# Kernel optimization log

Measured on AMD Instinct MI355X. Metric: run time of the kernel, lower is better.

The kernel has to match this reference:

```python
import jax, jax.numpy as jnp
import numpy as np

B = 65536          # number of 9-node graphs
NPG = 9            # nodes per graph (hardcoded in module)
N = B * NPG
D_IN, D_H = 11, 64
SOFTPLUS_BIAS = float(np.log(np.expm1(1.0)))  # biased_softplus_1.0 bias
SCALE_LB = 1e-4


def _make_edges():
    # fully connected (no self loops) within each 9-node graph
    pairs = np.array([(i, j) for i in range(NPG) for j in range(NPG) if i != j],
                     dtype=np.int64)  # [72, 2]
    offs = (np.arange(B, dtype=np.int64) * NPG)[:, None]
    src = (offs + pairs[None, :, 0]).ravel()
    dst = (offs + pairs[None, :, 1]).ravel()
    return jnp.asarray(np.stack([src, dst]))  # [2, E]


def setup_inputs() -> dict:
    key = jax.random.key(0)
    ks = jax.random.split(key, 12)
    s_in = 1.0 / np.sqrt(D_IN)
    s_h = 1.0 / np.sqrt(D_H)
    return {
        "x": jax.random.normal(ks[0], (N, D_IN), jnp.float32),
        "edge_index": _make_edges(),
        "W_in": jax.random.normal(ks[1], (D_H, D_IN), jnp.float32) * s_in,
        "b_in": jax.random.normal(ks[2], (D_H,), jnp.float32) * s_in,
        "W1_rel": jax.random.normal(ks[3], (D_H, D_H), jnp.float32) * s_h,
        "b1": jax.random.normal(ks[4], (D_H,), jnp.float32) * s_h,
        "W1_root": jax.random.normal(ks[5], (D_H, D_H), jnp.float32) * s_h,
        "W2_rel": jax.random.normal(ks[6], (D_H, D_H), jnp.float32) * s_h,
        "b2": jax.random.normal(ks[7], (D_H,), jnp.float32) * s_h,
        "W2_root": jax.random.normal(ks[8], (D_H, D_H), jnp.float32) * s_h,
        "W_head": jax.random.normal(ks[9], (8, D_H, 2), jnp.float32) * s_h,
        "b_head": jax.random.normal(ks[10], (8, 2), jnp.float32) * s_h,
    }


def _graph_conv(x, src, dst, W_rel, b_rel, W_root, n):
    # PyG GraphConv: lin_rel(sum_{j in N(i)} x_j) + lin_root(x_i)
    agg = jax.ops.segment_sum(x[src], dst, num_segments=n)  # scatter-add gather
    return agg @ W_rel.T + b_rel + x @ W_root.T


def reference(x, edge_index, W_in, b_in, W1_rel, b1, W1_root,
              W2_rel, b2, W2_root, W_head, b_head):
    n = x.shape[0]
    src, dst = edge_index[0], edge_index[1]
    h = x @ W_in.T + b_in                                   # [N, 64]
    h = jnp.tanh(_graph_conv(h, src, dst, W1_rel, b1, W1_root, n))
    h = jnp.tanh(_graph_conv(h, src, dst, W2_rel, b2, W2_root, n))
    hg = h.reshape(n // NPG, NPG, D_H)[:, 1:, :]            # drop node 0: [B, 8, 64]
    out = jnp.einsum('bnd,ndo->bno', hg, W_head) + b_head   # per-node head: [B, 8, 2]
    loc = out[..., 0]
    scale = jnp.maximum(jax.nn.softplus(out[..., 1] + SOFTPLUS_BIAS), SCALE_LB)
    return (loc, scale)
```

## Files before the change

kernel.cpp:

```cpp
#include <hip/hip_runtime.h>
#include <hip/hip_bf16.h>

#define NPG 9
#define DH 64
#define DIN 11
#define GPB 32
#define ROWS (GPB*NPG)
#define TPB 576
#define NGRAPH 65536
#define NBLK (NGRAPH/GPB)
#define OUT_HALF ((long long)NGRAPH*8)

typedef __attribute__((ext_vector_type(8))) short short8;
typedef __attribute__((ext_vector_type(4))) float f32x4;

__device__ float g_winT[DIN*DH];
__device__ short g_bfrag1[16*512];
__device__ short g_bfrag2[16*512];
__device__ short g_bfragH[2*512];

__device__ __forceinline__ short f2b(float f) {
  unsigned u = __builtin_bit_cast(unsigned, f);
  u += 0x7fffu + ((u >> 16) & 1u);
  return (short)(u >> 16);
}
__device__ __forceinline__ float b2f(short s) {
  unsigned u = ((unsigned)(unsigned short)s) << 16;
  return __builtin_bit_cast(float, u);
}
__device__ __forceinline__ float fast_tanh(float v) {
  float e = __expf(2.f*v);
  return 1.f - 2.f*__builtin_amdgcn_rcpf(e + 1.f);
}

__global__ void prep_kernel(const float* __restrict__ W_in,
                            const float* __restrict__ W1_rel, const float* __restrict__ W1_root,
                            const float* __restrict__ W2_rel, const float* __restrict__ W2_root,
                            const float* __restrict__ W_head) {
  int idx = blockIdx.x*blockDim.x + threadIdx.x;
  if (idx < DIN*DH) {
    int k = idx >> 6, f = idx & 63;
    g_winT[idx] = W_in[f*DIN + k];
  }
  if (idx < 16*512) {
    int frag = idx >> 9, kk = frag >> 2, nt = frag & 3;
    int l = (idx >> 3) & 63, j = idx & 7;
    int k2 = kk*32 + ((l >> 4) << 3) + j;
    int n  = nt*16 + (l & 15);
    float v1, v2;
    if (k2 < 64) {
      v1 = W1_root[n*DH + k2] - W1_rel[n*DH + k2];
      v2 = W2_root[n*DH + k2] - W2_rel[n*DH + k2];
    } else {
      v1 = W1_rel[n*DH + k2 - 64];
      v2 = W2_rel[n*DH + k2 - 64];
    }
    g_bfrag1[idx] = f2b(v1);
    g_bfrag2[idx] = f2b(v2);
  }
  if (idx < 2*512) {
    int kk = idx >> 9;
    int l = (idx >> 3) & 63, j = idx & 7;
    int k = kk*32 + ((l >> 4) << 3) + j;
    int n = l & 15;
    g_bfragH[idx] = f2b(W_head[(n >> 1)*(DH*2) + k*2 + (n & 1)]);
  }
}

#define HS_OFF(r, c) ((r)*64 + (((c) ^ ((r) & 7)) << 3))

__global__ __launch_bounds__(TPB) void fused_kernel(
    const float* __restrict__ x,
    const float* __restrict__ b_in,
    const float* __restrict__ b1,
    const float* __restrict__ b2,
    const float* __restrict__ bhead,
    float* __restrict__ out)
{
  __shared__ short Hs[ROWS*64];
  __shared__ union { float xs[ROWS*13]; short ss[GPB*64]; } u;

  const int tid  = threadIdx.x;
  const int lane = tid & 63;
  const int wave = tid >> 6;
  const int l15  = lane & 15;
  const int kgrp = lane >> 4;

  {
    const float* __restrict__ xsrc = x + (size_t)blockIdx.x * (ROWS*DIN);
    for (int i = tid; i < ROWS*DIN; i += TPB) {
      int r = (int)(((unsigned)i * 2979u) >> 15);
      int c = i - r*DIN;
      u.xs[r*13 + c] = xsrc[i];
    }
  }
  __syncthreads();

  if (tid < ROWS) {
    const int row = tid;
    float xr[DIN];
    #pragma unroll
    for (int k = 0; k < DIN; ++k) xr[k] = u.xs[row*13 + k];
    float z[DH];
    #pragma unroll
    for (int f = 0; f < DH; ++f) z[f] = b_in[f];
    #pragma unroll
    for (int k = 0; k < DIN; ++k) {
      const float s = xr[k];
      const float* __restrict__ w = &g_winT[k*DH];
      #pragma unroll
      for (int f = 0; f < DH; ++f) z[f] += s * w[f];
    }
    #pragma unroll
    for (int c = 0; c < 8; ++c) {
      short8 v;
      #pragma unroll
      for (int j = 0; j < 8; ++j) v[j] = f2b(z[c*8 + j]);
      *(short8*)&Hs[HS_OFF(row, c)] = v;
    }
  }
  __syncthreads();

  auto layer = [&](const short* __restrict__ bfrag, const float* __restrict__ bias) {
    if (tid < 256) {
      const int g = tid >> 3, fc = tid & 7;
      float s[8] = {0,0,0,0,0,0,0,0};
      #pragma unroll
      for (int j = 0; j < NPG; ++j) {
        const int r = g*NPG + j;
        short8 v = *(const short8*)&Hs[HS_OFF(r, fc)];
        #pragma unroll
        for (int e = 0; e < 8; ++e) s[e] += b2f(v[e]);
      }
      short8 o;
      #pragma unroll
      for (int e = 0; e < 8; ++e) o[e] = f2b(s[e]);
      *(short8*)&u.ss[g*64 + ((fc ^ (g & 7)) << 3)] = o;
    }
    __syncthreads();

    short8 B[4][4];
    #pragma unroll
    for (int kk = 0; kk < 4; ++kk)
      #pragma unroll
      for (int nt = 0; nt < 4; ++nt)
        B[kk][nt] = *(const short8*)&bfrag[((kk << 2) + nt)*512 + lane*8];

    float bias_c[4];
    #pragma unroll
    for (int nt = 0; nt < 4; ++nt) bias_c[nt] = bias[nt*16 + l15];

    f32x4 acc[2][4];
    #pragma unroll
    for (int tt = 0; tt < 2; ++tt)
      #pragma unroll
      for (int nt = 0; nt < 4; ++nt) acc[tt][nt] = (f32x4){0.f,0.f,0.f,0.f};

    #pragma unroll
    for (int tt = 0; tt < 2; ++tt) {
      const int row = (2*wave + tt)*16 + l15;
      const int g   = (row*57) >> 9;
      short8 A[4];
      #pragma unroll
      for (int kk = 0; kk < 2; ++kk)
        A[kk] = *(const short8*)&Hs[HS_OFF(row, kk*4 + kgrp)];
      #pragma unroll
      for (int kk = 2; kk < 4; ++kk)
        A[kk] = *(const short8*)&u.ss[g*64 + ((((kk - 2)*4 + kgrp) ^ (g & 7)) << 3)];
      #pragma unroll
      for (int kk = 0; kk < 4; ++kk)
        #pragma unroll
        for (int nt = 0; nt < 4; ++nt)
          acc[tt][nt] = __builtin_amdgcn_mfma_f32_16x16x32_bf16(A[kk], B[kk][nt], acc[tt][nt], 0, 0, 0);
    }
    __syncthreads();

    #pragma unroll
    for (int tt = 0; tt < 2; ++tt) {
      #pragma unroll
      for (int nt = 0; nt < 4; ++nt) {
        #pragma unroll
        for (int reg = 0; reg < 4; ++reg) {
          const int row = (2*wave + tt)*16 + kgrp*4 + reg;
          const int col = nt*16 + l15;
          float v = acc[tt][nt][reg] + bias_c[nt];
          v = fast_tanh(v);
          Hs[row*64 + (((col >> 3) ^ (row & 7)) << 3) + (col & 7)] = f2b(v);
        }
      }
    }
    __syncthreads();
  };

  layer(g_bfrag1, b1);
  layer(g_bfrag2, b2);

  short8 HB[2];
  #pragma unroll
  for (int kk = 0; kk < 2; ++kk)
    HB[kk] = *(const short8*)&g_bfragH[kk*512 + lane*8];

  const int p  = l15 >> 1;
  const int oc = l15 & 1;
  const float bh = bhead[p*2 + oc];

  #pragma unroll
  for (int tt = 0; tt < 2; ++tt) {
    const int t = 2*wave + tt;
    const int arow = t*16 + l15;
    f32x4 hacc = (f32x4){0.f,0.f,0.f,0.f};
    #pragma unroll
    for (int kk = 0; kk < 2; ++kk) {
      short8 A = *(const short8*)&Hs[HS_OFF(arow, kk*4 + kgrp)];
      hacc = __builtin_amdgcn_mfma_f32_16x16x32_bf16(A, HB[kk], hacc, 0, 0, 0);
    }
    #pragma unroll
    for (int reg = 0; reg < 4; ++reg) {
      const int row = t*16 + kgrp*4 + reg;
      const int g   = (row*57) >> 9;
      const int nn  = row - g*NPG;
      if (nn == p + 1) {
        const float v = hacc[reg] + bh;
        const long long gg = (long long)blockIdx.x * GPB + g;
        if (oc == 0) {
          out[gg*8 + p] = v;
        } else {
          float tv = v + 0.5413248546129181f;
          float e  = __expf(tv);
          float sp = (tv > 15.f) ? tv : __logf(1.f + e);
          out[OUT_HALF + gg*8 + p] = fmaxf(sp, 1e-4f);
        }
      }
    }
  }
}

extern "C" void kernel_launch(void* const* d_in, const int* in_sizes, int n_in,
                              void* d_out, int out_size, void* d_ws, size_t ws_size,
                              hipStream_t stream) {
  const float* x       = (const float*)d_in[0];
  const float* W_in    = (const float*)d_in[2];
  const float* b_in    = (const float*)d_in[3];
  const float* W1_rel  = (const float*)d_in[4];
  const float* b1      = (const float*)d_in[5];
  const float* W1_root = (const float*)d_in[6];
  const float* W2_rel  = (const float*)d_in[7];
  const float* b2      = (const float*)d_in[8];
  const float* W2_root = (const float*)d_in[9];
  const float* Whead   = (const float*)d_in[10];
  const float* bhead   = (const float*)d_in[11];
  float* out = (float*)d_out;

  hipLaunchKernelGGL(prep_kernel, dim3(32), dim3(256), 0, stream,
                     W_in, W1_rel, W1_root, W2_rel, W2_root, Whead);
  hipLaunchKernelGGL(fused_kernel, dim3(NBLK), dim3(TPB), 0, stream,
                     x, b_in, b1, b2, bhead, out);
}
```

Measured before the change: 227.2 us.

## Fold input projection into layer-1 weights and shrink blocks to 256 threads

Precomputes combined weights so the input linear layer and the first graph convolution collapse into one small MFMA on the 11-dim raw features plus per-graph feature sums, with a folded bias. This removes the per-row scalar 11x64 FMA projection and the first 64-dim aggregation. Blocks change to 28 graphs with 256 threads and launch bounds for four blocks per CU, with tail guards because 65536 is not divisible by 28. The prep kernel now runs as a single block doing serial 64-term dot products, and the input features are rounded to bf16 before the folded product, which may cost some accuracy.

```diff
diff --git a/kernel.cpp b/kernel.cpp
--- a/kernel.cpp
+++ b/kernel.cpp
@@ -4,25 +4,26 @@
 #define NPG 9
 #define DH 64
 #define DIN 11
-#define GPB 32
+#define GPB 28
 #define ROWS (GPB*NPG)
-#define TPB 576
+#define TPB 256
 #define NGRAPH 65536
-#define NBLK (NGRAPH/GPB)
+#define NROWTOT (NGRAPH*NPG)
+#define NBLK ((NGRAPH + GPB - 1)/GPB)
 #define OUT_HALF ((long long)NGRAPH*8)
 
 typedef __attribute__((ext_vector_type(8))) short short8;
+typedef __attribute__((ext_vector_type(4))) short short4v;
 typedef __attribute__((ext_vector_type(4))) float f32x4;
 
-__device__ float g_winT[DIN*DH];
-__device__ short g_bfrag1[16*512];
+__device__ float g_c1[DH];
+__device__ short g_bfrag1[4*512];
 __device__ short g_bfrag2[16*512];
 __device__ short g_bfragH[2*512];
 
-__device__ __forceinline__ short f2b(float f) {
-  unsigned u = __builtin_bit_cast(unsigned, f);
-  u += 0x7fffu + ((u >> 16) & 1u);
-  return (short)(u >> 16);
+__device__ __forceinline__ short f2bs(float f) {
+  __hip_bfloat16 h = __float2bfloat16(f);
+  return __builtin_bit_cast(short, h);
 }
 __device__ __forceinline__ float b2f(short s) {
   unsigned u = ((unsigned)(unsigned short)s) << 16;
@@ -33,52 +34,73 @@
   return 1.f - 2.f*__builtin_amdgcn_rcpf(e + 1.f);
 }
 
-__global__ void prep_kernel(const float* __restrict__ W_in,
-                            const float* __restrict__ W1_rel, const float* __restrict__ W1_root,
+__global__ void prep_kernel(const float* __restrict__ W_in, const float* __restrict__ b_in,
+                            const float* __restrict__ W1_rel, const float* __restrict__ b1,
+                            const float* __restrict__ W1_root,
                             const float* __restrict__ W2_rel, const float* __restrict__ W2_root,
                             const float* __restrict__ W_head) {
-  int idx = blockIdx.x*blockDim.x + threadIdx.x;
-  if (idx < DIN*DH) {
-    int k = idx >> 6, f = idx & 63;
-    g_winT[idx] = W_in[f*DIN + k];
-  }
-  if (idx < 16*512) {
-    int frag = idx >> 9, kk = frag >> 2, nt = frag & 3;
-    int l = (idx >> 3) & 63, j = idx & 7;
+  __shared__ float Wa[DH][DIN+1], Wb[DH][DIN+1];
+  const int tid = threadIdx.x;
+  for (int t = tid; t < DH*DIN; t += 1024) {
+    int n = t / DIN, k = t - n*DIN;
+    float a = 0.f, b = 0.f;
+    for (int m = 0; m < DH; ++m) {
+      float wi = W_in[m*DIN + k];
+      float r  = W1_rel[n*DH + m];
+      a += (W1_root[n*DH + m] - r) * wi;
+      b += r * wi;
+    }
+    Wa[n][k] = a; Wb[n][k] = b;
+  }
+  if (tid < DH) {
+    float c = b1[tid];
+    for (int m = 0; m < DH; ++m)
+      c += (W1_root[tid*DH + m] + 8.f*W1_rel[tid*DH + m]) * b_in[m];
+    g_c1[tid] = c;
+  }
+  __syncthreads();
+  for (int i = tid; i < 4*512; i += 1024) {
+    int nt = i >> 9;
+    int l = (i >> 3) & 63, j = i & 7;
+    int k = ((l >> 4) << 3) + j;
+    int n = nt*16 + (l & 15);
+    float v = 0.f;
+    if (k < 16) { if (k < DIN) v = Wa[n][k]; }
+    else        { if (k - 16 < DIN) v = Wb[n][k - 16]; }
+    g_bfrag1[i] = f2bs(v);
+  }
+  for (int i = tid; i < 16*512; i += 1024) {
+    int frag = i >> 9, kk = frag >> 2, nt = frag & 3;
+    int l = (i >> 3) & 63, j = i & 7;
     int k2 = kk*32 + ((l >> 4) << 3) + j;
     int n  = nt*16 + (l & 15);
-    float v1, v2;
-    if (k2 < 64) {
-      v1 = W1_root[n*DH + k2] - W1_rel[n*DH + k2];
-      v2 = W2_root[n*DH + k2] - W2_rel[n*DH + k2];
-    } else {
-      v1 = W1_rel[n*DH + k2 - 64];
-      v2 = W2_rel[n*DH + k2 - 64];
-    }
-    g_bfrag1[idx] = f2b(v1);
-    g_bfrag2[idx] = f2b(v2);
-  }
-  if (idx < 2*512) {
-    int kk = idx >> 9;
-    int l = (idx >> 3) & 63, j = idx & 7;
+    float v = (k2 < 64) ? (W2_root[n*DH + k2] - W2_rel[n*DH + k2])
+                        : W2_rel[n*DH + k2 - 64];
+    g_bfrag2[i] = f2bs(v);
+  }
+  for (int i = tid; i < 2*512; i += 1024) {
+    int kk = i >> 9;
+    int l = (i >> 3) & 63, j = i & 7;
     int k = kk*32 + ((l >> 4) << 3) + j;
     int n = l & 15;
-    g_bfragH[idx] = f2b(W_head[(n >> 1)*(DH*2) + k*2 + (n & 1)]);
-  }
-}
-
-#define HS_OFF(r, c) ((r)*64 + (((c) ^ ((r) & 7)) << 3))
-
-__global__ __launch_bounds__(TPB) void fused_kernel(
+    g_bfragH[i] = f2bs(W_head[(n >> 1)*(DH*2) + k*2 + (n & 1)]);
+  }
+}
+
+#define HS_W(r, col) ((r)*64 + (((((col) >> 3)) ^ ((r) & 7)) << 3) + ((col) & 7))
+#define HS_CH(r, c)  ((r)*64 + (((c) ^ ((r) & 7)) << 3))
+
+__global__ __launch_bounds__(TPB, 4) void fused_kernel(
     const float* __restrict__ x,
-    const float* __restrict__ b_in,
-    const float* __restrict__ b1,
     const float* __restrict__ b2,
     const float* __restrict__ bhead,
     float* __restrict__ out)
 {
-  __shared__ short Hs[ROWS*64];
-  __shared__ union { float xs[ROWS*13]; short ss[GPB*64]; } u;
+  __shared__ short Hs[ROWS*DH];
+  __shared__ union {
+    struct { short xs[ROWS*12]; short Sx[GPB*12]; } a;
+    short ss[GPB*64];
+  } U;
 
   const int tid  = threadIdx.x;
   const int lane = tid & 63;
@@ -86,149 +108,185 @@
   const int l15  = lane & 15;
   const int kgrp = lane >> 4;
 
+  short* xs = U.a.xs;
+  short* Sx = U.a.Sx;
+  short* ss = U.ss;
+
   {
-    const float* __restrict__ xsrc = x + (size_t)blockIdx.x * (ROWS*DIN);
-    for (int i = tid; i < ROWS*DIN; i += TPB) {
+    const long long base = (long long)blockIdx.x * (ROWS*DIN);
+    long long rem = (long long)NROWTOT*DIN - base;
+    const int lim = rem < (ROWS*DIN) ? (int)rem : (ROWS*DIN);
+    for (int i = tid; i < lim; i += TPB) {
       int r = (int)(((unsigned)i * 2979u) >> 15);
       int c = i - r*DIN;
-      u.xs[r*13 + c] = xsrc[i];
-    }
-  }
-  __syncthreads();
-
-  if (tid < ROWS) {
-    const int row = tid;
-    float xr[DIN];
-    #pragma unroll
-    for (int k = 0; k < DIN; ++k) xr[k] = u.xs[row*13 + k];
-    float z[DH];
-    #pragma unroll
-    for (int f = 0; f < DH; ++f) z[f] = b_in[f];
-    #pragma unroll
-    for (int k = 0; k < DIN; ++k) {
-      const float s = xr[k];
-      const float* __restrict__ w = &g_winT[k*DH];
-      #pragma unroll
-      for (int f = 0; f < DH; ++f) z[f] += s * w[f];
-    }
-    #pragma unroll
-    for (int c = 0; c < 8; ++c) {
-      short8 v;
-      #pragma unroll
-      for (int j = 0; j < 8; ++j) v[j] = f2b(z[c*8 + j]);
-      *(short8*)&Hs[HS_OFF(row, c)] = v;
-    }
-  }
-  __syncthreads();
-
-  auto layer = [&](const short* __restrict__ bfrag, const float* __restrict__ bias) {
-    if (tid < 256) {
-      const int g = tid >> 3, fc = tid & 7;
-      float s[8] = {0,0,0,0,0,0,0,0};
-      #pragma unroll
-      for (int j = 0; j < NPG; ++j) {
-        const int r = g*NPG + j;
-        short8 v = *(const short8*)&Hs[HS_OFF(r, fc)];
+      xs[r*12 + c] = f2bs(x[base + i]);
+    }
+    if (tid < ROWS) xs[tid*12 + 11] = 0;
+  }
+  __syncthreads();
+
+  if (tid < GPB*2) {
+    const int g = tid >> 1, half = tid & 1;
+    const int rbase = g*NPG;
+    float s[8] = {0,0,0,0,0,0,0,0};
+    for (int j = 0; j < NPG; ++j) {
+      const short* p = &xs[(rbase + j)*12 + half*8];
+      short4v a = *(const short4v*)p;
+      short4v b = *(const short4v*)(p + 4);
+      s[0] += b2f(a[0]); s[1] += b2f(a[1]); s[2] += b2f(a[2]); s[3] += b2f(a[3]);
+      s[4] += b2f(b[0]); s[5] += b2f(b[1]); s[6] += b2f(b[2]); s[7] += b2f(b[3]);
+    }
+    short4v o0;
+    o0[0] = f2bs(s[0]); o0[1] = f2bs(s[1]); o0[2] = f2bs(s[2]); o0[3] = f2bs(s[3]);
+    *(short4v*)&Sx[g*12 + half*8] = o0;
+    if (!half) {
+      short4v o1;
+      o1[0] = f2bs(s[4]); o1[1] = f2bs(s[5]); o1[2] = f2bs(s[6]); o1[3] = f2bs(s[7]);
+      *(short4v*)&Sx[g*12 + 4] = o1;
+    }
+  }
+  __syncthreads();
+
+  {
+    short8 B1[4];
+    #pragma unroll
+    for (int nt = 0; nt < 4; ++nt) B1[nt] = *(const short8*)&g_bfrag1[nt*512 + lane*8];
+    float c1v[4];
+    #pragma unroll
+    for (int nt = 0; nt < 4; ++nt) c1v[nt] = g_c1[nt*16 + l15];
+
+    const int sel = kgrp & 1;
+    #pragma unroll
+    for (int i = 0; i < 4; ++i) {
+      const int t = wave*4 + i;
+      int row = t*16 + l15; if (row > ROWS-1) row = ROWS-1;
+      const int g = (row*57) >> 9;
+      const short* bp = (kgrp < 2) ? &xs[row*12] : &Sx[g*12];
+      short4v lo = *(const short4v*)(bp + sel*8);
+      short4v hi = *(const short4v*)(bp + 4);
+      short8 A;
+      A[0] = lo[0]; A[1] = lo[1]; A[2] = lo[2]; A[3] = lo[3];
+      A[4] = sel ? (short)0 : hi[0];
+      A[5] = sel ? (short)0 : hi[1];
+      A[6] = sel ? (short)0 : hi[2];
+      A[7] = sel ? (short)0 : hi[3];
+      f32x4 acc[4];
+      #pragma unroll
+      for (int nt = 0; nt < 4; ++nt)
+        acc[nt] = (f32x4){c1v[nt], c1v[nt], c1v[nt], c1v[nt]};
+      #pragma unroll
+      for (int nt = 0; nt < 4; ++nt)
+        acc[nt] = __builtin_amdgcn_mfma_f32_16x16x32_bf16(A, B1[nt], acc[nt], 0, 0, 0);
+      #pragma unroll
+      for (int nt = 0; nt < 4; ++nt) {
         #pragma unroll
-        for (int e = 0; e < 8; ++e) s[e] += b2f(v[e]);
+        for (int reg = 0; reg < 4; ++reg) {
+          const int orow = t*16 + kgrp*4 + reg;
+          if (orow < ROWS) {
+            const int col = nt*16 + l15;
+            Hs[HS_W(orow, col)] = f2bs(fast_tanh(acc[nt][reg]));
+          }
+        }
       }
-      short8 o;
-      #pragma unroll
-      for (int e = 0; e < 8; ++e) o[e] = f2b(s[e]);
-      *(short8*)&u.ss[g*64 + ((fc ^ (g & 7)) << 3)] = o;
-    }
-    __syncthreads();
-
-    short8 B[4][4];
+    }
+  }
+  __syncthreads();
+
+  if (tid < GPB*8) {
+    const int fc = (int)(((unsigned)tid * 2341u) >> 16);
+    const int g  = tid - fc*GPB;
+    float s[8] = {0,0,0,0,0,0,0,0};
+    for (int j = 0; j < NPG; ++j) {
+      const int r = g*NPG + j;
+      short8 v = *(const short8*)&Hs[HS_CH(r, fc)];
+      #pragma unroll
+      for (int e = 0; e < 8; ++e) s[e] += b2f(v[e]);
+    }
+    short8 o;
+    #pragma unroll
+    for (int e = 0; e < 8; ++e) o[e] = f2bs(s[e]);
+    *(short8*)&ss[g*64 + ((fc ^ (g & 7)) << 3)] = o;
+  }
+  __syncthreads();
+
+  {
+    short8 B2[4][4];
     #pragma unroll
     for (int kk = 0; kk < 4; ++kk)
       #pragma unroll
       for (int nt = 0; nt < 4; ++nt)
-        B[kk][nt] = *(const short8*)&bfrag[((kk << 2) + nt)*512 + lane*8];
-
-    float bias_c[4];
-    #pragma unroll
-    for (int nt = 0; nt < 4; ++nt) bias_c[nt] = bias[nt*16 + l15];
-
-    f32x4 acc[2][4];
-    #pragma unroll
-    for (int tt = 0; tt < 2; ++tt)
-      #pragma unroll
-      for (int nt = 0; nt < 4; ++nt) acc[tt][nt] = (f32x4){0.f,0.f,0.f,0.f};
-
-    #pragma unroll
-    for (int tt = 0; tt < 2; ++tt) {
-      const int row = (2*wave + tt)*16 + l15;
-      const int g   = (row*57) >> 9;
+        B2[kk][nt] = *(const short8*)&g_bfrag2[((kk << 2) + nt)*512 + lane*8];
+    float b2v[4];
+    #pragma unroll
+    for (int nt = 0; nt < 4; ++nt) b2v[nt] = b2[nt*16 + l15];
+
+    #pragma unroll
+    for (int i = 0; i < 4; ++i) {
+      const int t = wave*4 + i;
+      int row = t*16 + l15; if (row > ROWS-1) row = ROWS-1;
+      const int g = (row*57) >> 9;
       short8 A[4];
-      #pragma unroll
-      for (int kk = 0; kk < 2; ++kk)
-        A[kk] = *(const short8*)&Hs[HS_OFF(row, kk*4 + kgrp)];
-      #pragma unroll
-      for (int kk = 2; kk < 4; ++kk)
-        A[kk] = *(const short8*)&u.ss[g*64 + ((((kk - 2)*4 + kgrp) ^ (g & 7)) << 3)];
+      A[0] = *(const short8*)&Hs[HS_CH(row, 0 + kgrp)];
+      A[1] = *(const short8*)&Hs[HS_CH(row, 4 + kgrp)];
+      A[2] = *(const short8*)&ss[g*64 + (((0 + kgrp) ^ (g & 7)) << 3)];
+      A[3] = *(const short8*)&ss[g*64 + (((4 + kgrp) ^ (g & 7)) << 3)];
+      f32x4 acc[4];
+      #pragma unroll
+      for (int nt = 0; nt < 4; ++nt)
+        acc[nt] = (f32x4){b2v[nt], b2v[nt], b2v[nt], b2v[nt]};
       #pragma unroll
       for (int kk = 0; kk < 4; ++kk)
         #pragma unroll
         for (int nt = 0; nt < 4; ++nt)
-          acc[tt][nt] = __builtin_amdgcn_mfma_f32_16x16x32_bf16(A[kk], B[kk][nt], acc[tt][nt], 0, 0, 0);
-    }
-    __syncthreads();
-
-    #pragma unroll
-    for (int tt = 0; tt < 2; ++tt) {
+          acc[nt] = __builtin_amdgcn_mfma_f32_16x16x32_bf16(A[kk], B2[kk][nt], acc[nt], 0, 0, 0);
       #pragma unroll
       for (int nt = 0; nt < 4; ++nt) {
         #pragma unroll
         for (int reg = 0; reg < 4; ++reg) {
-          const int row = (2*wave + tt)*16 + kgrp*4 + reg;
-          const int col = nt*16 + l15;
-          float v = acc[tt][nt][reg] + bias_c[nt];
-          v = fast_tanh(v);
-          Hs[row*64 + (((col >> 3) ^ (row & 7)) << 3) + (col & 7)] = f2b(v);
+          const int orow = t*16 + kgrp*4 + reg;
+          if (orow < ROWS) {
+            const int col = nt*16 + l15;
+            Hs[HS_W(orow, col)] = f2bs(fast_tanh(acc[nt][reg]));
+          }
         }
       }
     }
-    __syncthreads();
-  };
-
-  layer(g_bfrag1, b1);
-  layer(g_bfrag2, b2);
-
-  short8 HB[2];
-  #pragma unroll
-  for (int kk = 0; kk < 2; ++kk)
-    HB[kk] = *(const short8*)&g_bfragH[kk*512 + lane*8];
-
-  const int p  = l15 >> 1;
-  const int oc = l15 & 1;
-  const float bh = bhead[p*2 + oc];
-
-  #pragma unroll
-  for (int tt = 0; tt < 2; ++tt) {
-    const int t = 2*wave + tt;
-    const int arow = t*16 + l15;
-    f32x4 hacc = (f32x4){0.f,0.f,0.f,0.f};
-    #pragma unroll
-    for (int kk = 0; kk < 2; ++kk) {
-      short8 A = *(const short8*)&Hs[HS_OFF(arow, kk*4 + kgrp)];
-      hacc = __builtin_amdgcn_mfma_f32_16x16x32_bf16(A, HB[kk], hacc, 0, 0, 0);
-    }
-    #pragma unroll
-    for (int reg = 0; reg < 4; ++reg) {
-      const int row = t*16 + kgrp*4 + reg;
-      const int g   = (row*57) >> 9;
-      const int nn  = row - g*NPG;
-      if (nn == p + 1) {
-        const float v = hacc[reg] + bh;
-        const long long gg = (long long)blockIdx.x * GPB + g;
-        if (oc == 0) {
-          out[gg*8 + p] = v;
-        } else {
-          float tv = v + 0.5413248546129181f;
-          float e  = __expf(tv);
-          float sp = (tv > 15.f) ? tv : __logf(1.f + e);
-          out[OUT_HALF + gg*8 + p] = fmaxf(sp, 1e-4f);
+  }
+  __syncthreads();
+
+  {
+    short8 HB0 = *(const short8*)&g_bfragH[lane*8];
+    short8 HB1 = *(const short8*)&g_bfragH[512 + lane*8];
+    const int p  = l15 >> 1;
+    const int oc = l15 & 1;
+    const float bh = bhead[p*2 + oc];
+    #pragma unroll
+    for (int i = 0; i < 4; ++i) {
+      const int t = wave*4 + i;
+      int row = t*16 + l15; if (row > ROWS-1) row = ROWS-1;
+      short8 A0 = *(const short8*)&Hs[HS_CH(row, 0 + kgrp)];
+      short8 A1 = *(const short8*)&Hs[HS_CH(row, 4 + kgrp)];
+      f32x4 acc = (f32x4){bh, bh, bh, bh};
+      acc = __builtin_amdgcn_mfma_f32_16x16x32_bf16(A0, HB0, acc, 0, 0, 0);
+      acc = __builtin_amdgcn_mfma_f32_16x16x32_bf16(A1, HB1, acc, 0, 0, 0);
+      #pragma unroll
+      for (int reg = 0; reg < 4; ++reg) {
+        const int orow = t*16 + kgrp*4 + reg;
+        if (orow < ROWS) {
+          const int g  = (orow*57) >> 9;
+          const int nn = orow - g*NPG;
+          const long long gg = (long long)blockIdx.x*GPB + g;
+          if (nn == p + 1 && gg < NGRAPH) {
+            const float v = acc[reg];
+            if (oc == 0) {
+              out[gg*8 + p] = v;
+            } else {
+              float tv = v + 0.5413248546129181f;
+              float e  = __expf(tv);
+              float sp = (tv > 15.f) ? tv : __logf(1.f + e);
+              out[OUT_HALF + gg*8 + p] = fmaxf(sp, 1e-4f);
+            }
+          }
         }
       }
     }
@@ -251,8 +309,8 @@
   const float* bhead   = (const float*)d_in[11];
   float* out = (float*)d_out;
 
-  hipLaunchKernelGGL(prep_kernel, dim3(32), dim3(256), 0, stream,
-                     W_in, W1_rel, W1_root, W2_rel, W2_root, Whead);
+  hipLaunchKernelGGL(prep_kernel, dim3(1), dim3(1024), 0, stream,
+                     W_in, b_in, W1_rel, b1, W1_root, W2_rel, W2_root, Whead);
   hipLaunchKernelGGL(fused_kernel, dim3(NBLK), dim3(TPB), 0, stream,
-                     x, b_in, b1, b2, bhead, out);
-}
+                     x, b2, bhead, out);
+}
```

Result: no change. 226.7 us (-0.2%).
